# Kernel tuning notes

Hardware: AMD Instinct MI355X
Metric: run time of the kernel (lower is better)

## Reference

```python
import jax, jax.numpy as jnp
import numpy as np

FLOAT_INF = -1000.0


def setup_inputs() -> dict:
    key = jax.random.key(0)
    k1, k2, k3, k4 = jax.random.split(key, 4)
    N, L, C = 512, 1024, 128
    start_tag, end_tag = C - 2, C - 1
    logits = jax.random.normal(k1, (N, L, C), dtype=jnp.float32)
    transition = jax.random.normal(k2, (C, C), dtype=jnp.float32)
    transition = transition.at[:, end_tag].set(FLOAT_INF)
    transition = transition.at[start_tag, :].set(FLOAT_INF)
    labels = jax.random.randint(k3, (N, L), 0, C - 2)  # real labels only (no START/END)
    lengths = jax.random.randint(k4, (N,), L // 2, L + 1)
    mask = jnp.arange(L)[None, :] < lengths[:, None]  # bool (N, L), True = real token
    return {"logits": logits, "transition": transition, "labels": labels,
            "mask": mask, "start_tag": start_tag, "end_tag": end_tag}


def reference(logits, transition, labels, mask, start_tag, end_tag):
    """CRF negative log-likelihood per sample: forward_alg - get_sentence_score. Shape (N,)."""
    N, L, C = logits.shape
    maskf = mask.astype(logits.dtype)

    # ---- sentence score s(X, y) = sum A[y_i, y_{i+1}] + sum P[i, y_i] ----
    start_col = jnp.full((N, 1), start_tag, dtype=labels.dtype)
    end_col = jnp.full((N, 1), end_tag, dtype=labels.dtype)
    lab_ext = jnp.concatenate([start_col, labels, end_col], axis=1)  # (N, L+2)
    ones_b = jnp.ones((N, 1), dtype=bool)
    mask_se = jnp.concatenate([ones_b, mask, ones_b], axis=1)        # (N, L+2)
    lab_ext = jnp.where(mask_se, lab_ext, end_tag)  # padding labels -> END
    # transition[next_label, prev_label], matching torch gather(row=labels_r, col=labels_l)
    trans_pair = transition[lab_ext[:, 1:], lab_ext[:, :-1]]         # (N, L+1)
    mask_s = jnp.concatenate([jnp.ones((N, 1), logits.dtype), maskf], axis=1)
    trans_score = jnp.sum(trans_pair * mask_s, axis=1)               # (N,)
    emis = jnp.take_along_axis(logits, labels[:, :, None], axis=2)[..., 0]
    emis_score = jnp.sum(emis * maskf, axis=1)                       # (N,)
    sent_score = trans_score + emis_score

    # ---- forward algorithm: log sum over all paths, fused as a lax.scan ----
    alpha0 = jnp.full((N, C), FLOAT_INF, dtype=logits.dtype).at[:, start_tag].set(0.0)
    logits_t = jnp.swapaxes(logits, 0, 1)  # (L, N, C)
    mask_t = jnp.swapaxes(mask, 0, 1)      # (L, N)

    def step(alpha, xs):
        logit, m = xs
        # scores[n, next, prev] = alpha[n, prev] + A[next, prev] + P[n, next]
        scores = alpha[:, None, :] + transition[None, :, :] + logit[:, :, None]
        new = jax.scipy.special.logsumexp(scores, axis=2)  # (N, C)
        alpha = jnp.where(m[:, None], new, alpha)
        return alpha, None

    alpha, _ = jax.lax.scan(step, alpha0, (logits_t, mask_t))
    total = jax.scipy.special.logsumexp(alpha + transition[end_tag][None, :], axis=1)  # (N,)

    return total - sent_score
```

## Files before the change

kernel.cpp:

```cpp
#include <hip/hip_runtime.h>
#include <stdint.h>

#define C_ 128

typedef __attribute__((ext_vector_type(8))) short short8;
typedef __attribute__((ext_vector_type(4))) float f32x4;
typedef __attribute__((ext_vector_type(4))) unsigned int u32x4;

__device__ __forceinline__ unsigned short f2bf(float x){
  unsigned u = __builtin_bit_cast(unsigned, x);
  return (unsigned short)((u + 0x7FFFu + ((u >> 16) & 1u)) >> 16);
}
__device__ __forceinline__ float bf2f(unsigned short h){
  unsigned u = ((unsigned)h) << 16;
  return __builtin_bit_cast(float, u);
}
__device__ __forceinline__ unsigned cvtpk(float lo, float hi){
  unsigned r;
  asm("v_cvt_pk_bf16_f32 %0, %1, %2" : "=v"(r) : "v"(lo), "v"(hi));
  return r;
}
__device__ __forceinline__ void bar(){
  asm volatile("s_waitcnt lgkmcnt(0)" ::: "memory");
  __builtin_amdgcn_s_barrier();
  asm volatile("" ::: "memory");
}

__device__ __forceinline__ bool mask_is_i32(const void* mask){
  return ((const unsigned*)mask)[0] == 1u;
}

__global__ __launch_bounds__(512, 1) void crf_scan(
    const float* __restrict__ logits,
    const float* __restrict__ trans,
    const int*   __restrict__ labels,
    const void*  __restrict__ mask,
    float* __restrict__ out,
    int L,
    const int* __restrict__ startp, const int* __restrict__ endp)
{
  __shared__ unsigned st[2 * 1024];
  __shared__ float mred[16][8];
  __shared__ float sent_lds[16];

  const int tid = threadIdx.x;
  const int w   = tid >> 6;
  const int l   = tid & 63;
  const int lj  = l & 15;
  const int lg  = l >> 4;
  const int j0  = 16 * w + 4 * lg;
  const int n0  = blockIdx.x * 16;
  const int start_tag = *startp;
  const int end_tag   = *endp;
  const bool i32m = mask_is_i32(mask);
  const float LN2 = 0.69314718055994530942f;

  int cnt = 0;
  {
    const int seg = L >> 2;
    if (i32m) {
      const int4* m4 = (const int4*)((const int*)mask + (size_t)(n0 + lj) * L + lg * seg);
      for (int i = 0; i < (seg >> 2); i++) {
        int4 v = m4[i];
        cnt += (v.x != 0) + (v.y != 0) + (v.z != 0) + (v.w != 0);
      }
    } else {
      const unsigned* mr = (const unsigned*)((const unsigned char*)mask + (size_t)(n0 + lj) * L + lg * seg);
      for (int i = 0; i < (seg >> 2); i++) cnt += __popc(mr[i]);
    }
    cnt += __shfl_xor(cnt, 16);
    cnt += __shfl_xor(cnt, 32);
  }
  const int len_n = cnt;
  int mn = len_n;
  mn = min(mn, __shfl_xor(mn, 1));
  mn = min(mn, __shfl_xor(mn, 2));
  mn = min(mn, __shfl_xor(mn, 4));
  mn = min(mn, __shfl_xor(mn, 8));
  const int T_main = (mn - 3) & ~3;

  {
    const int s = tid >> 5;
    const int g = tid & 31;
    const int*  lab  = labels + (size_t)(n0 + s) * L;
    const float* lrow = logits + (size_t)(n0 + s) * L * C_;
    const int*           m32 = (const int*)mask + (size_t)(n0 + s) * L;
    const unsigned char* m8  = (const unsigned char*)mask + (size_t)(n0 + s) * L;
    float acc = 0.f;
    for (int t = g; t < L; t += 32) {
      int mt = i32m ? m32[t] : (int)m8[t];
      if (mt) {
        int lt  = lab[t];
        int mnx = (t + 1 < L) ? (i32m ? m32[t + 1] : (int)m8[t + 1]) : 0;
        int nxt = mnx ? lab[t + 1] : end_tag;
        acc += lrow[(size_t)t * C_ + lt] + trans[(size_t)nxt * C_ + lt];
      }
    }
    #pragma unroll
    for (int m = 1; m < 32; m <<= 1) acc += __shfl_xor(acc, m);
    if (g == 0) sent_lds[s] = acc + trans[(size_t)lab[0] * C_ + start_tag];
  }

  short8 af[4];
  #pragma unroll
  for (int ks = 0; ks < 4; ks++) {
    const float* tp = trans + (size_t)(16 * w + lj) * C_ + 32 * ks + 8 * lg;
    f32x4 e0 = *(const f32x4*)tp;
    f32x4 e1 = *(const f32x4*)(tp + 4);
    short8 f;
    #pragma unroll
    for (int i = 0; i < 4; i++) f[i] = (short)f2bf(expf(e0[i]));
    #pragma unroll
    for (int i = 0; i < 4; i++) f[4 + i] = (short)f2bf(expf(e1[i]));
    af[ks] = f;
  }

  ((u32x4*)st)[tid] = (u32x4){0, 0, 0, 0};
  bar();
  if (tid < 16) {
    int phys = ((start_tag >> 3) ^ tid) & 15;
    st[tid * 64 + phys * 4 + ((start_tag & 7) >> 1)] =
        (start_tag & 1) ? 0x3F800000u : 0x00003F80u;
  }
  bar();

  unsigned prev0 = 0, prev1 = 0;
  #pragma unroll
  for (int i = 0; i < 4; i++)
    if (j0 + i == start_tag) {
      if (i == 0) prev0 |= 0x3F80u;
      if (i == 1) prev0 |= 0x3F80u << 16;
      if (i == 2) prev1 |= 0x3F80u;
      if (i == 3) prev1 |= 0x3F80u << 16;
    }

  const int wr_off = lj * 64 + ((((2 * w + (lg >> 1)) ^ lj) & 15) << 2) + ((lg & 1) << 1);
  const int rd0 = lj * 64 + ((((0 + lg) ^ lj) & 15) << 2);
  const int rd1 = lj * 64 + ((((4 + lg) ^ lj) & 15) << 2);
  const int rd2 = lj * 64 + ((((8 + lg) ^ lj) & 15) << 2);
  const int rd3 = lj * 64 + ((((12 + lg) ^ lj) & 15) << 2);

  const float L2E = 1.44269504088896340736f;
  const float NC  = -8.0f * L2E;

  const float* lbase = logits + (size_t)(n0 + lj) * L * C_ + j0;
  f32x4 lv0, lv1, lv2, lv3;
  asm volatile("global_load_dwordx4 %0, %1, off" : "=v"(lv0) : "v"(lbase));
  asm volatile("global_load_dwordx4 %0, %1, off" : "=v"(lv1) : "v"(lbase + C_));
  asm volatile("global_load_dwordx4 %0, %1, off" : "=v"(lv2) : "v"(lbase + 2 * C_));

  float pc0, pc1, pc2, pc3;
  asm volatile("s_waitcnt vmcnt(2)" ::: "memory");
  __builtin_amdgcn_sched_barrier(0);
  pc0 = __builtin_amdgcn_exp2f(fmaf(lv0[0], L2E, NC));
  pc1 = __builtin_amdgcn_exp2f(fmaf(lv0[1], L2E, NC));
  pc2 = __builtin_amdgcn_exp2f(fmaf(lv0[2], L2E, NC));
  pc3 = __builtin_amdgcn_exp2f(fmaf(lv0[3], L2E, NC));

  float lm = 0.f;

#define SCAN_STEP(T, LVNXT, LVISS, CUR, TAILF)                                    \
  {                                                                               \
    const unsigned* sc = st + (CUR) * 1024;                                       \
    u32x4 b0 = *(const u32x4*)&sc[rd0];                                           \
    u32x4 b1 = *(const u32x4*)&sc[rd1];                                           \
    u32x4 b2 = *(const u32x4*)&sc[rd2];                                           \
    u32x4 b3 = *(const u32x4*)&sc[rd3];                                           \
    {              \
      int ts = TAILF ? min((T) + 3, L - 1) : ((T) + 3);                           \
      const float* lp = lbase + (size_t)ts * C_;                                  \
      asm volatile("global_load_dwordx4 %0, %1, off" : "=v"(LVISS) : "v"(lp));    \
    }                                                                             \
    asm volatile("s_waitcnt vmcnt(2)" ::: "memory");        \
    __builtin_amdgcn_sched_barrier(0);                                            \
             \
    float pn0 = __builtin_amdgcn_exp2f(fmaf(LVNXT[0], L2E, NC));                  \
    float pn1 = __builtin_amdgcn_exp2f(fmaf(LVNXT[1], L2E, NC));                  \
    float pn2 = __builtin_amdgcn_exp2f(fmaf(LVNXT[2], L2E, NC));                  \
    float pn3 = __builtin_amdgcn_exp2f(fmaf(LVNXT[3], L2E, NC));                  \
    f32x4 z = {0.f, 0.f, 0.f, 0.f};                                               \
    f32x4 a0 = __builtin_amdgcn_mfma_f32_16x16x32_bf16(af[0], __builtin_bit_cast(short8, b0), z, 0, 0, 0); \
    f32x4 a1 = __builtin_amdgcn_mfma_f32_16x16x32_bf16(af[1], __builtin_bit_cast(short8, b1), z, 0, 0, 0); \
    f32x4 a2 = __builtin_amdgcn_mfma_f32_16x16x32_bf16(af[2], __builtin_bit_cast(short8, b2), z, 0, 0, 0); \
    f32x4 a3 = __builtin_amdgcn_mfma_f32_16x16x32_bf16(af[3], __builtin_bit_cast(short8, b3), z, 0, 0, 0); \
    float wv0 = ((a0[0] + a1[0]) + (a2[0] + a3[0])) * pc0;                        \
    float wv1 = ((a0[1] + a1[1]) + (a2[1] + a3[1])) * pc1;                        \
    float wv2 = ((a0[2] + a1[2]) + (a2[2] + a3[2])) * pc2;                        \
    float wv3 = ((a0[3] + a1[3]) + (a2[3] + a3[3])) * pc3;                        \
    if (((T) & 7) == 7) {                                                         \
      float tm = fmaxf(fmaxf(wv0, wv1), fmaxf(wv2, wv3));                         \
      tm = fmaxf(tm, __shfl_xor(tm, 16));                                         \
      tm = fmaxf(tm, __shfl_xor(tm, 32));                                         \
      if (lg == 0) mred[lj][w] = tm;                                              \
      bar();                                                                      \
      f32x4 ma = *(const f32x4*)&mred[lj][0];                                     \
      f32x4 mb = *(const f32x4*)&mred[lj][4];                                     \
      float m = fmaxf(fmaxf(fmaxf(ma[0], ma[1]), fmaxf(ma[2], ma[3])),            \
                      fmaxf(fmaxf(mb[0], mb[1]), fmaxf(mb[2], mb[3])));           \
      float rm = __builtin_amdgcn_rcpf(m);                                        \
      wv0 *= rm; wv1 *= rm; wv2 *= rm; wv3 *= rm;                                 \
      if (!(TAILF) || (T) < len_n) lm += LN2 * __builtin_amdgcn_logf(m);          \
    }                                                                             \
    unsigned pk0 = cvtpk(wv0, wv1);                                               \
    unsigned pk1 = cvtpk(wv2, wv3);                                               \
    if (TAILF) {                                                                  \
      bool alive = (T) < len_n;                                                   \
      pk0 = alive ? pk0 : prev0;                                                  \
      pk1 = alive ? pk1 : prev1;                                                  \
    }                                                                             \
    *(unsigned long long*)&st[((CUR) ^ 1) * 1024 + wr_off] =                      \
        ((unsigned long long)pk1 << 32) | pk0;                                    \
    prev0 = pk0; prev1 = pk1;                                                     \
    pc0 = pn0; pc1 = pn1; pc2 = pn2; pc3 = pn3;                                   \
    bar();                                                                        \
  }

  for (int t = 0; t < T_main; t += 4) {
    SCAN_STEP(t,     lv1, lv3, 0, false);
    SCAN_STEP(t + 1, lv2, lv0, 1, false);
    SCAN_STEP(t + 2, lv3, lv1, 0, false);
    SCAN_STEP(t + 3, lv0, lv2, 1, false);
  }
  for (int t = T_main; t < L; t += 4) {
    SCAN_STEP(t,     lv1, lv3, 0, true);
    SCAN_STEP(t + 1, lv2, lv0, 1, true);
    SCAN_STEP(t + 2, lv3, lv1, 0, true);
    SCAN_STEP(t + 3, lv0, lv2, 1, true);
  }
#undef SCAN_STEP

  {
    const float* te = trans + (size_t)end_tag * C_ + j0;
    float es = bf2f((unsigned short)(prev0 & 0xffff)) * expf(te[0])
             + bf2f((unsigned short)(prev0 >> 16))    * expf(te[1])
             + bf2f((unsigned short)(prev1 & 0xffff)) * expf(te[2])
             + bf2f((unsigned short)(prev1 >> 16))    * expf(te[3]);
    es += __shfl_xor(es, 16);
    es += __shfl_xor(es, 32);
    if (lg == 0) mred[lj][w] = es;
    bar();
    if (w == 0 && lg == 0) {
      f32x4 a = *(const f32x4*)&mred[lj][0];
      f32x4 b = *(const f32x4*)&mred[lj][4];
      float S = ((a[0] + a[1]) + (a[2] + a[3])) + ((b[0] + b[1]) + (b[2] + b[3]));
      float total = 8.0f * (float)len_n + lm + LN2 * __builtin_amdgcn_logf(S);
      out[n0 + lj] = total - sent_lds[lj];
    }
  }
}

extern "C" void kernel_launch(void* const* d_in, const int* in_sizes, int n_in,
                              void* d_out, int out_size, void* d_ws, size_t ws_size,
                              hipStream_t stream) {
  const float* logits = (const float*)d_in[0];
  const float* trans  = (const float*)d_in[1];
  const int*   labels = (const int*)d_in[2];
  const void*  mask   = (const void*)d_in[3];
  const int* startp = (const int*)d_in[4];
  const int* endp   = (const int*)d_in[5];
  float* out  = (float*)d_out;

  const int N = out_size;
  const int L = in_sizes[2] / N;

  crf_scan<<<N / 16, 512, 0, stream>>>(logits, trans, labels, mask, out, L, startp, endp);
}
```

Measured before the change: 398.2 us.

## Offload sentence-score computation to separate blocks synchronized via flags

Splits the sentence-score gather (emission and transition sums) off the scan blocks into 32 extra blocks that write results to workspace and signal through release/acquire flags. The scan blocks then start the forward recurrence immediately and only wait on the flag at the final output. This takes the serial gather prologue off the critical path of the 32 scan blocks, at the cost of an extra memset launch, a workspace dependency, and a spin-wait that assumes all 64 blocks are co-resident.

```diff
diff --git a/kernel.cpp b/kernel.cpp
--- a/kernel.cpp
+++ b/kernel.cpp
@@ -30,58 +30,29 @@
   return ((const unsigned*)mask)[0] == 1u;
 }
 
-__global__ __launch_bounds__(512, 1) void crf_scan(
+__global__ __launch_bounds__(512, 1) void crf_fused(
     const float* __restrict__ logits,
     const float* __restrict__ trans,
     const int*   __restrict__ labels,
     const void*  __restrict__ mask,
+    float* __restrict__ ws_sent,
+    int*   __restrict__ flags,
     float* __restrict__ out,
     int L,
     const int* __restrict__ startp, const int* __restrict__ endp)
 {
-  __shared__ unsigned st[2 * 1024];
-  __shared__ float mred[16][8];
-  __shared__ float sent_lds[16];
-
+  const int bid = blockIdx.x;
   const int tid = threadIdx.x;
-  const int w   = tid >> 6;
-  const int l   = tid & 63;
-  const int lj  = l & 15;
-  const int lg  = l >> 4;
-  const int j0  = 16 * w + 4 * lg;
-  const int n0  = blockIdx.x * 16;
   const int start_tag = *startp;
   const int end_tag   = *endp;
   const bool i32m = mask_is_i32(mask);
   const float LN2 = 0.69314718055994530942f;
 
-  int cnt = 0;
-  {
-    const int seg = L >> 2;
-    if (i32m) {
-      const int4* m4 = (const int4*)((const int*)mask + (size_t)(n0 + lj) * L + lg * seg);
-      for (int i = 0; i < (seg >> 2); i++) {
-        int4 v = m4[i];
-        cnt += (v.x != 0) + (v.y != 0) + (v.z != 0) + (v.w != 0);
-      }
-    } else {
-      const unsigned* mr = (const unsigned*)((const unsigned char*)mask + (size_t)(n0 + lj) * L + lg * seg);
-      for (int i = 0; i < (seg >> 2); i++) cnt += __popc(mr[i]);
-    }
-    cnt += __shfl_xor(cnt, 16);
-    cnt += __shfl_xor(cnt, 32);
-  }
-  const int len_n = cnt;
-  int mn = len_n;
-  mn = min(mn, __shfl_xor(mn, 1));
-  mn = min(mn, __shfl_xor(mn, 2));
-  mn = min(mn, __shfl_xor(mn, 4));
-  mn = min(mn, __shfl_xor(mn, 8));
-  const int T_main = (mn - 3) & ~3;
-
-  {
-    const int s = tid >> 5;
-    const int g = tid & 31;
+  if (bid >= 32) {
+    const int pb = bid - 32;
+    const int n0 = pb * 16;
+    const int s  = tid >> 5;
+    const int g  = tid & 31;
     const int*  lab  = labels + (size_t)(n0 + s) * L;
     const float* lrow = logits + (size_t)(n0 + s) * L * C_;
     const int*           m32 = (const int*)mask + (size_t)(n0 + s) * L;
@@ -98,8 +69,48 @@
     }
     #pragma unroll
     for (int m = 1; m < 32; m <<= 1) acc += __shfl_xor(acc, m);
-    if (g == 0) sent_lds[s] = acc + trans[(size_t)lab[0] * C_ + start_tag];
-  }
+    if (g == 0) ws_sent[n0 + s] = acc + trans[(size_t)lab[0] * C_ + start_tag];
+    __syncthreads();
+    if (tid == 0) {
+      __threadfence();
+      __hip_atomic_store(&flags[pb], 1, __ATOMIC_RELEASE, __HIP_MEMORY_SCOPE_AGENT);
+    }
+    return;
+  }
+
+  __shared__ unsigned st[2 * 1024];
+  __shared__ float mred[16][8];
+
+  const int w   = tid >> 6;
+  const int l   = tid & 63;
+  const int lj  = l & 15;
+  const int lg  = l >> 4;
+  const int j0  = 16 * w + 4 * lg;
+  const int n0  = bid * 16;
+
+  int cnt = 0;
+  {
+    const int seg = L >> 2;
+    if (i32m) {
+      const int4* m4 = (const int4*)((const int*)mask + (size_t)(n0 + lj) * L + lg * seg);
+      for (int i = 0; i < (seg >> 2); i++) {
+        int4 v = m4[i];
+        cnt += (v.x != 0) + (v.y != 0) + (v.z != 0) + (v.w != 0);
+      }
+    } else {
+      const unsigned* mr = (const unsigned*)((const unsigned char*)mask + (size_t)(n0 + lj) * L + lg * seg);
+      for (int i = 0; i < (seg >> 2); i++) cnt += __popc(mr[i]);
+    }
+    cnt += __shfl_xor(cnt, 16);
+    cnt += __shfl_xor(cnt, 32);
+  }
+  const int len_n = cnt;
+  int mn = len_n;
+  mn = min(mn, __shfl_xor(mn, 1));
+  mn = min(mn, __shfl_xor(mn, 2));
+  mn = min(mn, __shfl_xor(mn, 4));
+  mn = min(mn, __shfl_xor(mn, 8));
+  const int T_main = (mn - 3) & ~3;
 
   short8 af[4];
   #pragma unroll
@@ -240,11 +251,14 @@
     if (lg == 0) mred[lj][w] = es;
     bar();
     if (w == 0 && lg == 0) {
+      while (__hip_atomic_load(&flags[bid], __ATOMIC_ACQUIRE,
+                               __HIP_MEMORY_SCOPE_AGENT) == 0)
+        __builtin_amdgcn_s_sleep(8);
       f32x4 a = *(const f32x4*)&mred[lj][0];
       f32x4 b = *(const f32x4*)&mred[lj][4];
       float S = ((a[0] + a[1]) + (a[2] + a[3])) + ((b[0] + b[1]) + (b[2] + b[3]));
       float total = 8.0f * (float)len_n + lm + LN2 * __builtin_amdgcn_logf(S);
-      out[n0 + lj] = total - sent_lds[lj];
+      out[n0 + lj] = total - ws_sent[n0 + lj];
     }
   }
 }
@@ -263,5 +277,10 @@
   const int N = out_size;
   const int L = in_sizes[2] / N;
 
-  crf_scan<<<N / 16, 512, 0, stream>>>(logits, trans, labels, mask, out, L, startp, endp);
-}
+  float* ws_sent = (float*)d_ws;
+  int*   flags   = (int*)((char*)d_ws + 2048);
+
+  hipMemsetAsync(flags, 0, 32 * sizeof(int), stream);
+  crf_fused<<<64, 512, 0, stream>>>(logits, trans, labels, mask,
+                                    ws_sent, flags, out, L, startp, endp);
+}
```

Measured after the change: 347.6 us. 1.15x faster.
